# Kernel optimization log

Hardware: AMD Instinct MI355X
Metric: run time of the kernel (lower is better)

## Reference

```python
import jax, jax.numpy as jnp
import numpy as np

D_MODEL = 1024
HEADS = 16
Q_DIM = 1024
HEAD_DIM = Q_DIM // HEADS


def setup_inputs() -> dict:
    key = jax.random.key(0)
    ks = jax.random.split(key, 9)
    B, S = 2, 2048
    scale = 1.0 / np.sqrt(D_MODEL)
    inp = {
        "embeddings": jax.random.normal(ks[0], (B, S, D_MODEL), dtype=jnp.float32),
        "Wq": jax.random.normal(ks[1], (D_MODEL, Q_DIM), dtype=jnp.float32) * scale,
        "bq": jnp.zeros((Q_DIM,), dtype=jnp.float32),
        "Wk": jax.random.normal(ks[2], (D_MODEL, Q_DIM), dtype=jnp.float32) * scale,
        "bk": jnp.zeros((Q_DIM,), dtype=jnp.float32),
        "Wv": jax.random.normal(ks[3], (D_MODEL, Q_DIM), dtype=jnp.float32) * scale,
        "bv": jnp.zeros((Q_DIM,), dtype=jnp.float32),
        "Wo": jax.random.normal(ks[4], (Q_DIM, D_MODEL), dtype=jnp.float32) * scale,
        "bo": jnp.zeros((D_MODEL,), dtype=jnp.float32),
    }
    return inp


def reference(embeddings, Wq, bq, Wk, bk, Wv, bv, Wo, bo):
    B, S, _ = embeddings.shape
    # projections -> [B, H, S, Dh]
    def proj(W, b):
        x = embeddings @ W + b
        return x.reshape(B, S, HEADS, HEAD_DIM).transpose(0, 2, 1, 3)
    q = proj(Wq, bq)
    k = proj(Wk, bk)
    v = proj(Wv, bv)
    # scores scaled by sqrt(head_dim) as in source (no mask, dropout is no-op)
    scores = jnp.einsum("bhqd,bhkd->bhqk", q, k) / jnp.sqrt(
        jnp.asarray(HEAD_DIM, dtype=q.dtype)
    )
    p = jax.nn.softmax(scores, axis=-1)
    attn = jnp.einsum("bhqk,bhkd->bhqd", p, v)
    attn = attn.transpose(0, 2, 1, 3).reshape(B, S, Q_DIM)
    return attn @ Wo + bo
```

## Files before the change

### kernel.cpp

```cpp
#include <hip/hip_runtime.h>
#include <hip/hip_bf16.h>

#define BB 2
#define SS 2048
#define DMODEL 1024
#define NHEADS 16
#define DHEAD 64
#define MTOT (BB*SS)
#define NQKV 3072
#define QSCALE 0.18033688011112042f

typedef short bh8 __attribute__((ext_vector_type(8)));
typedef float fx4 __attribute__((ext_vector_type(4)));

__device__ __forceinline__ short f2bs(float f) {
    __hip_bfloat16 h = __float2bfloat16(f);
    return *reinterpret_cast<short*>(&h);
}

__device__ __forceinline__ void gload_lds16(const short* g, short* l) {
    __builtin_amdgcn_global_load_lds(
        (const __attribute__((address_space(1))) unsigned int*)g,
        (__attribute__((address_space(3))) unsigned int*)l, 16, 0, 0);
}

__global__ __launch_bounds__(256) void cvt_emb(const float* __restrict__ x,
                                               short* __restrict__ y, int n) {
    int i = (blockIdx.x * 256 + threadIdx.x) * 4;
    if (i + 3 < n) {
        float4 v = *(const float4*)(x + i);
        short4 o;
        o.x = f2bs(v.x); o.y = f2bs(v.y); o.z = f2bs(v.z); o.w = f2bs(v.w);
        *(short4*)(y + i) = o;
    }
}

__global__ __launch_bounds__(256) void transpose_w(
        const float* __restrict__ Wq, const float* __restrict__ Wk,
        const float* __restrict__ Wv, const float* __restrict__ Wo,
        short* __restrict__ Wt_qkv, short* __restrict__ Wot) {
    __shared__ float tile[64][65];
    int z = blockIdx.z;
    const float* src = (z == 0) ? Wq : (z == 1) ? Wk : (z == 2) ? Wv : Wo;
    short* dst = (z == 3) ? Wot : (Wt_qkv + (size_t)z * 1024 * 1024);
    int n0 = blockIdx.x * 64, k0 = blockIdx.y * 64;
    int tx = threadIdx.x, ty = threadIdx.y;
    for (int j = 0; j < 16; j++) {
        int r = ty + j * 4;
        tile[r][tx] = src[(size_t)(k0 + r) * 1024 + n0 + tx];
    }
    __syncthreads();
    for (int j = 0; j < 16; j++) {
        int r = ty + j * 4;
        dst[(size_t)(n0 + r) * 1024 + k0 + tx] = f2bs(tile[tx][r]);
    }
}

template<int BM, int BN, int NN, int MODE>
__global__ __launch_bounds__(256) void gemm_bt_t(
        const short* __restrict__ A, const short* __restrict__ Bt,
        const float* __restrict__ bq, const float* __restrict__ bk,
        const float* __restrict__ bv, const float* __restrict__ bo,
        short* __restrict__ Qout, short* __restrict__ Kout,
        short* __restrict__ Vtout, float* __restrict__ Cout) {
    const int K = 1024;
    constexpr int ROWS = BM + BN;
    constexpr int CPW  = ROWS / 64;
    constexpr int MBK  = MTOT / BM;
    constexpr int STRIP = MBK / 8;
    constexpr int MT = BM / 32, NT = BN / 32;
    __shared__ __align__(16) short S[3][ROWS * 32];

    int tid = threadIdx.x;
    int w = tid >> 6, l = tid & 63, quad = l >> 4, ln = l & 15;
    int wm = w & 1, wn = w >> 1;

    int id = blockIdx.x;
    int xcd = id & 7, local = id >> 3;
    int mi = xcd * STRIP + (local % STRIP);
    int ni = local / STRIP;
    int m0 = mi * BM, n0 = ni * BN;

    const short* gsrc[CPW];
    int loff[CPW];
    #pragma unroll
    for (int j = 0; j < CPW; j++) {
        int r0 = (w * CPW + j) * 16;
        int row = r0 + (l >> 2);
        gsrc[j] = (r0 < BM ? A + (size_t)(m0 + row) * K
                           : Bt + (size_t)(n0 + row - BM) * K) + (l & 3) * 8;
        loff[j] = r0 * 32;
    }

    short *sC = &S[0][0], *sN = &S[1][0], *sN2 = &S[2][0];
    #pragma unroll
    for (int j = 0; j < CPW; j++) gload_lds16(gsrc[j], sC + loff[j]);
    #pragma unroll
    for (int j = 0; j < CPW; j++) gload_lds16(gsrc[j] + 32, sN + loff[j]);

    fx4 acc[MT][NT] = {};
    for (int it = 0; it < 32; ++it) {
        if (it < 31) {
            if constexpr (CPW == 4)
                asm volatile("s_waitcnt vmcnt(4)\n\ts_barrier" ::: "memory");
            else
                asm volatile("s_waitcnt vmcnt(3)\n\ts_barrier" ::: "memory");
        } else {
            asm volatile("s_waitcnt vmcnt(0)\n\ts_barrier" ::: "memory");
        }
        if (it < 30) {
            int k0 = (it + 2) * 32;
            #pragma unroll
            for (int j = 0; j < CPW; j++) gload_lds16(gsrc[j] + k0, sN2 + loff[j]);
        }
        bh8 af[MT], bf[NT];
        #pragma unroll
        for (int mt = 0; mt < MT; mt++)
            af[mt] = *(const bh8*)&sC[(wm * (BM / 2) + mt * 16 + ln) * 32 + quad * 8];
        #pragma unroll
        for (int nt = 0; nt < NT; nt++)
            bf[nt] = *(const bh8*)&sC[(BM + wn * (BN / 2) + nt * 16 + ln) * 32 + quad * 8];
        #pragma unroll
        for (int mt = 0; mt < MT; mt++)
            #pragma unroll
            for (int nt = 0; nt < NT; nt++)
                acc[mt][nt] = __builtin_amdgcn_mfma_f32_16x16x32_bf16(af[mt], bf[nt], acc[mt][nt], 0, 0, 0);
        short* t;
        t = sC; sC = sN; sN = sN2; sN2 = t;
    }

    #pragma unroll
    for (int mt = 0; mt < MT; mt++) {
        #pragma unroll
        for (int nt = 0; nt < NT; nt++) {
            int n = n0 + wn * (BN / 2) + nt * 16 + ln;
            int mbase = m0 + wm * (BM / 2) + mt * 16 + quad * 4;
            #pragma unroll
            for (int r = 0; r < 4; r++) {
                float v = acc[mt][nt][r];
                int m = mbase + r;
                if constexpr (MODE == 0) {
                    int which = n >> 10, nn = n & 1023, h = nn >> 6, d = nn & 63;
                    float bias = (which == 0) ? bq[nn] : (which == 1) ? bk[nn] : bv[nn];
                    v += bias;
                    int b = m >> 11, s = m & 2047;
                    if (which == 0)
                        Qout[(((size_t)(b * 16 + h) * 2048) + s) * 64 + d] = f2bs(v * QSCALE);
                    else if (which == 1)
                        Kout[(((size_t)(b * 16 + h) * 2048) + s) * 64 + d] = f2bs(v);
                    else
                        Vtout[((size_t)(b * 16 + h) * 64 + d) * 2048 + s] = f2bs(v);
                } else {
                    Cout[(size_t)m * 1024 + n] = v + bo[n];
                }
            }
        }
    }
}

__global__ __launch_bounds__(256, 4) void flash_attn(
        const short* __restrict__ Q, const short* __restrict__ Kg,
        const short* __restrict__ Vt,
        float* __restrict__ O0, float* __restrict__ O1,
        float* __restrict__ L0, float* __restrict__ L1) {
    __shared__ __align__(16) short Ks[64 * 64];
    __shared__ __align__(16) short Vs[64 * 64];
    __shared__ __align__(16) short Ps[4][32 * 68];

    int tid = threadIdx.x;
    int w = tid >> 6, l = tid & 63, quad = l >> 4, ln = l & 15;
    int id = blockIdx.x;
    int xcd = id & 7, local = id >> 3;
    int bh = xcd * 4 + (local & 3);
    int t = local >> 2;
    int qx = t & 15, z = t >> 4;
    int qblk = qx * 128 + w * 32;
    const short* Qb = Q  + (size_t)bh * 2048 * 64;
    const short* Kb = Kg + (size_t)bh * 2048 * 64 + (size_t)z * 1024 * 64;
    const short* Vb = Vt + (size_t)bh * 64 * 2048 + z * 1024;
    float* Op = z ? O1 : O0;
    float* Lp = z ? L1 : L0;
    int swz = ln & 7;

    bh8 qf[2][2];
    #pragma unroll
    for (int qt = 0; qt < 2; qt++)
        #pragma unroll
        for (int c = 0; c < 2; c++)
            qf[qt][c] = *(const bh8*)&Qb[(size_t)(qblk + qt * 16 + ln) * 64 + c * 32 + quad * 8];

    int srow = tid >> 2, sp0 = tid & 3;
    int kw0 = srow * 64 + ((sp0 ^ (srow & 7)) * 8);
    int kw1 = srow * 64 + (((sp0 + 4) ^ (srow & 7)) * 8);
    const short* gK = Kb + (size_t)srow * 64;
    const short* gV = Vb + (size_t)srow * 2048;

    {
        uint4 a = *(const uint4*)(gK + sp0 * 8);
        uint4 bb = *(const uint4*)(gK + (sp0 + 4) * 8);
        uint4 c = *(const uint4*)(gV + sp0 * 8);
        uint4 d = *(const uint4*)(gV + (sp0 + 4) * 8);
        *(uint4*)&Ks[kw0] = a; *(uint4*)&Ks[kw1] = bb;
        *(uint4*)&Vs[kw0] = c; *(uint4*)&Vs[kw1] = d;
    }
    asm volatile("s_waitcnt lgkmcnt(0)\n\ts_barrier" ::: "memory");

    fx4 o[2][4] = {};
    float lpart[2] = {0.f, 0.f};

    for (int it = 0; it < 16; ++it) {
        uint4 ra, rb, rc, rd;
        bool pre = (it < 15);
        if (pre) {
            const short* gk = gK + (size_t)(it + 1) * 4096;
            const short* gv = gV + (size_t)(it + 1) * 64;
            ra = *(const uint4*)(gk + sp0 * 8);
            rb = *(const uint4*)(gk + (sp0 + 4) * 8);
            rc = *(const uint4*)(gv + sp0 * 8);
            rd = *(const uint4*)(gv + (sp0 + 4) * 8);
        }

        fx4 s[2][4] = {};
        #pragma unroll
        for (int mt = 0; mt < 4; mt++) {
            bh8 kf0 = *(const bh8*)&Ks[(mt * 16 + ln) * 64 + ((quad ^ swz) * 8)];
            bh8 kf1 = *(const bh8*)&Ks[(mt * 16 + ln) * 64 + (((quad + 4) ^ swz) * 8)];
            #pragma unroll
            for (int qt = 0; qt < 2; qt++) {
                s[qt][mt] = __builtin_amdgcn_mfma_f32_16x16x32_bf16(kf0, qf[qt][0], s[qt][mt], 0, 0, 0);
                s[qt][mt] = __builtin_amdgcn_mfma_f32_16x16x32_bf16(kf1, qf[qt][1], s[qt][mt], 0, 0, 0);
            }
        }

        #pragma unroll
        for (int qt = 0; qt < 2; qt++) {
            #pragma unroll
            for (int mt = 0; mt < 4; mt++) {
                float p0 = __builtin_amdgcn_exp2f(s[qt][mt][0]);
                float p1 = __builtin_amdgcn_exp2f(s[qt][mt][1]);
                float p2 = __builtin_amdgcn_exp2f(s[qt][mt][2]);
                float p3 = __builtin_amdgcn_exp2f(s[qt][mt][3]);
                lpart[qt] += (p0 + p1) + (p2 + p3);
                union { __hip_bfloat162 h2[2]; short4 s4; } u;
                u.h2[0] = __float22bfloat162_rn(make_float2(p0, p1));
                u.h2[1] = __float22bfloat162_rn(make_float2(p2, p3));
                *(short4*)&Ps[w][(qt * 16 + ln) * 64 +
                                 (((mt * 2 + (quad >> 1)) ^ swz) * 8) + (quad & 1) * 4] = u.s4;
            }
        }
        asm volatile("s_waitcnt lgkmcnt(0)" ::: "memory");

        #pragma unroll
        for (int c2 = 0; c2 < 2; c2++) {
            bh8 pf0 = *(const bh8*)&Ps[w][(0 * 16 + ln) * 64 + (((c2 * 4 + quad) ^ swz) * 8)];
            bh8 pf1 = *(const bh8*)&Ps[w][(1 * 16 + ln) * 64 + (((c2 * 4 + quad) ^ swz) * 8)];
            #pragma unroll
            for (int dt = 0; dt < 4; dt++) {
                bh8 vf = *(const bh8*)&Vs[(dt * 16 + ln) * 64 + (((c2 * 4 + quad) ^ swz) * 8)];
                o[0][dt] = __builtin_amdgcn_mfma_f32_16x16x32_bf16(vf, pf0, o[0][dt], 0, 0, 0);
                o[1][dt] = __builtin_amdgcn_mfma_f32_16x16x32_bf16(vf, pf1, o[1][dt], 0, 0, 0);
            }
        }

        asm volatile("s_barrier" ::: "memory");
        if (pre) {
            *(uint4*)&Ks[kw0] = ra; *(uint4*)&Ks[kw1] = rb;
            *(uint4*)&Vs[kw0] = rc; *(uint4*)&Vs[kw1] = rd;
        }
        asm volatile("s_waitcnt lgkmcnt(0)\n\ts_barrier" ::: "memory");
    }

    float* PsF = (float*)&Ps[w][0];
    int row = l >> 2, seg = l & 3;
    #pragma unroll
    for (int qt = 0; qt < 2; qt++) {
        #pragma unroll
        for (int dt = 0; dt < 4; dt++)
            *(fx4*)&PsF[ln * 68 + dt * 16 + quad * 4] = o[qt][dt];
        asm volatile("s_waitcnt lgkmcnt(0)" ::: "memory");
        float* orow = &Op[((size_t)bh * 2048 + qblk + qt * 16 + row) * 64];
        #pragma unroll
        for (int j = 0; j < 4; j++) {
            fx4 v = *(fx4*)&PsF[row * 68 + seg * 16 + j * 4];
            *(fx4*)&orow[seg * 16 + j * 4] = v;
        }
        asm volatile("s_waitcnt lgkmcnt(0)" ::: "memory");
        float lr = lpart[qt];
        lr += __shfl_xor(lr, 16);
        lr += __shfl_xor(lr, 32);
        if (l < 16) Lp[(size_t)bh * 2048 + qblk + qt * 16 + l] = lr;
    }
}

__global__ __launch_bounds__(256) void combine(
        const float* __restrict__ O0, const float* __restrict__ O1,
        const float* __restrict__ L0, const float* __restrict__ L1,
        short* __restrict__ Ctx) {
    int t = blockIdx.x * 256 + threadIdx.x;
    size_t base = (size_t)t * 8;
    int bhq = t >> 3;
    int d = (t & 7) * 8;
    int bh = bhq >> 11, q = bhq & 2047;
    int b = bh >> 4, h = bh & 15;
    float inv = 1.0f / (L0[bhq] + L1[bhq]);
    float4 a0 = *(const float4*)(O0 + base);
    float4 a1 = *(const float4*)(O0 + base + 4);
    float4 c0 = *(const float4*)(O1 + base);
    float4 c1 = *(const float4*)(O1 + base + 4);
    union { short s[8]; bh8 v; } o;
    o.s[0] = f2bs((a0.x + c0.x) * inv); o.s[1] = f2bs((a0.y + c0.y) * inv);
    o.s[2] = f2bs((a0.z + c0.z) * inv); o.s[3] = f2bs((a0.w + c0.w) * inv);
    o.s[4] = f2bs((a1.x + c1.x) * inv); o.s[5] = f2bs((a1.y + c1.y) * inv);
    o.s[6] = f2bs((a1.z + c1.z) * inv); o.s[7] = f2bs((a1.w + c1.w) * inv);
    *(bh8*)&Ctx[((size_t)(b * 2048 + q)) * 1024 + h * 64 + d] = o.v;
}

extern "C" void kernel_launch(void* const* d_in, const int* in_sizes, int n_in,
                              void* d_out, int out_size, void* d_ws, size_t ws_size,
                              hipStream_t stream) {
    const float* emb = (const float*)d_in[0];
    const float* Wq  = (const float*)d_in[1];
    const float* bq  = (const float*)d_in[2];
    const float* Wk  = (const float*)d_in[3];
    const float* bk  = (const float*)d_in[4];
    const float* Wv  = (const float*)d_in[5];
    const float* bv  = (const float*)d_in[6];
    const float* Wo  = (const float*)d_in[7];
    const float* bo  = (const float*)d_in[8];

    char* ws = (char*)d_ws;
    const size_t MB = 1024 * 1024;
    short* Xbf  = (short*)(ws + 0);
    short* Wt   = (short*)(ws + 8 * MB);
    float* Op1  = (float*)(ws + 0);
    short* Wot  = (short*)(ws + 17 * MB);
    short* Qb   = (short*)(ws + 19 * MB);
    short* Ctx  = (short*)(ws + 19 * MB);
    short* Kb   = (short*)(ws + 27 * MB);
    short* Vtb  = (short*)(ws + 35 * MB);
    float* L0   = (float*)(ws + 43 * MB);
    float* L1   = (float*)(ws + 43 * MB + 256 * 1024);
    float* Op0  = (float*)d_out;

    cvt_emb<<<4096, 256, 0, stream>>>(emb, Xbf, MTOT * DMODEL);
    transpose_w<<<dim3(16, 16, 4), dim3(64, 4), 0, stream>>>(Wq, Wk, Wv, Wo, Wt, Wot);
    gemm_bt_t<128, 128, NQKV, 0><<<768, 256, 0, stream>>>(
        Xbf, Wt, bq, bk, bv, nullptr, Qb, Kb, Vtb, nullptr);
    flash_attn<<<1024, 256, 0, stream>>>(Qb, Kb, Vtb, Op0, Op1, L0, L1);
    combine<<<2048, 256, 0, stream>>>(Op0, Op1, L0, L1, Ctx);
    gemm_bt_t<64, 128, DMODEL, 1><<<512, 256, 0, stream>>>(
        Ctx, Wot, nullptr, nullptr, nullptr, bo, nullptr, nullptr, nullptr, (float*)d_out);
}
```

Baseline: 207.7 us.

## Double-buffer K/V tiles with direct global-to-LDS loads in flash attention

Replaces the register-staged K/V prefetch with double-buffered LDS tiles filled by global_load_lds. Each wave loads its own 16 rows with a source-side XOR swizzle, so each iteration needs one vmcnt wait and barrier instead of two barriers plus register-to-LDS stores. V fragments are hoisted into registers before the softmax. The P staging buffer is halved by processing one 16-row query tile at a time. The epilogue reuses the K/V LDS region for output staging; this adds LDS footprint and register pressure, which may reduce occupancy.

```diff
diff --git a/kernel.cpp b/kernel.cpp
--- a/kernel.cpp
+++ b/kernel.cpp
@@ -163,9 +163,9 @@
         const short* __restrict__ Vt,
         float* __restrict__ O0, float* __restrict__ O1,
         float* __restrict__ L0, float* __restrict__ L1) {
-    __shared__ __align__(16) short Ks[64 * 64];
-    __shared__ __align__(16) short Vs[64 * 64];
-    __shared__ __align__(16) short Ps[4][32 * 68];
+    __shared__ __align__(16) short Ks[2][64 * 64];
+    __shared__ __align__(16) short Vs[2][64 * 64];
+    __shared__ __align__(16) short Ps[4][16 * 64];
 
     int tid = threadIdx.x;
     int w = tid >> 6, l = tid & 63, quad = l >> 4, ln = l & 15;
@@ -189,48 +189,55 @@
         for (int c = 0; c < 2; c++)
             qf[qt][c] = *(const bh8*)&Qb[(size_t)(qblk + qt * 16 + ln) * 64 + c * 32 + quad * 8];
 
-    int srow = tid >> 2, sp0 = tid & 3;
-    int kw0 = srow * 64 + ((sp0 ^ (srow & 7)) * 8);
-    int kw1 = srow * 64 + (((sp0 + 4) ^ (srow & 7)) * 8);
-    const short* gK = Kb + (size_t)srow * 64;
-    const short* gV = Vb + (size_t)srow * 2048;
-
-    {
-        uint4 a = *(const uint4*)(gK + sp0 * 8);
-        uint4 bb = *(const uint4*)(gK + (sp0 + 4) * 8);
-        uint4 c = *(const uint4*)(gV + sp0 * 8);
-        uint4 d = *(const uint4*)(gV + (sp0 + 4) * 8);
-        *(uint4*)&Ks[kw0] = a; *(uint4*)&Ks[kw1] = bb;
-        *(uint4*)&Vs[kw0] = c; *(uint4*)&Vs[kw1] = d;
-    }
-    asm volatile("s_waitcnt lgkmcnt(0)\n\ts_barrier" ::: "memory");
+    int r0 = w * 16;
+    int rowA = r0 + (l >> 3), rowB = rowA + 8;
+    int posn = l & 7;
+    const short* gKa = Kb + (size_t)rowA * 64   + ((posn ^ (rowA & 7)) * 8);
+    const short* gKc = Kb + (size_t)rowB * 64   + ((posn ^ (rowB & 7)) * 8);
+    const short* gVa = Vb + (size_t)rowA * 2048 + ((posn ^ (rowA & 7)) * 8);
+    const short* gVc = Vb + (size_t)rowB * 2048 + ((posn ^ (rowB & 7)) * 8);
+
+    gload_lds16(gKa, &Ks[0][r0 * 64]);
+    gload_lds16(gKc, &Ks[0][(r0 + 8) * 64]);
+    gload_lds16(gVa, &Vs[0][r0 * 64]);
+    gload_lds16(gVc, &Vs[0][(r0 + 8) * 64]);
 
     fx4 o[2][4] = {};
     float lpart[2] = {0.f, 0.f};
 
     for (int it = 0; it < 16; ++it) {
-        uint4 ra, rb, rc, rd;
-        bool pre = (it < 15);
-        if (pre) {
-            const short* gk = gK + (size_t)(it + 1) * 4096;
-            const short* gv = gV + (size_t)(it + 1) * 64;
-            ra = *(const uint4*)(gk + sp0 * 8);
-            rb = *(const uint4*)(gk + (sp0 + 4) * 8);
-            rc = *(const uint4*)(gv + sp0 * 8);
-            rd = *(const uint4*)(gv + (sp0 + 4) * 8);
-        }
+        asm volatile("s_waitcnt vmcnt(0)\n\ts_barrier" ::: "memory");
+        int cur = it & 1;
+        if (it < 15) {
+            int nb = cur ^ 1;
+            size_t ko = (size_t)(it + 1) * 4096;
+            size_t vo = (size_t)(it + 1) * 64;
+            gload_lds16(gKa + ko, &Ks[nb][r0 * 64]);
+            gload_lds16(gKc + ko, &Ks[nb][(r0 + 8) * 64]);
+            gload_lds16(gVa + vo, &Vs[nb][r0 * 64]);
+            gload_lds16(gVc + vo, &Vs[nb][(r0 + 8) * 64]);
+        }
+        const short* KsB = Ks[cur];
+        const short* VsB = Vs[cur];
 
         fx4 s[2][4] = {};
         #pragma unroll
         for (int mt = 0; mt < 4; mt++) {
-            bh8 kf0 = *(const bh8*)&Ks[(mt * 16 + ln) * 64 + ((quad ^ swz) * 8)];
-            bh8 kf1 = *(const bh8*)&Ks[(mt * 16 + ln) * 64 + (((quad + 4) ^ swz) * 8)];
+            bh8 kf0 = *(const bh8*)&KsB[(mt * 16 + ln) * 64 + ((quad ^ swz) * 8)];
+            bh8 kf1 = *(const bh8*)&KsB[(mt * 16 + ln) * 64 + (((quad + 4) ^ swz) * 8)];
             #pragma unroll
             for (int qt = 0; qt < 2; qt++) {
                 s[qt][mt] = __builtin_amdgcn_mfma_f32_16x16x32_bf16(kf0, qf[qt][0], s[qt][mt], 0, 0, 0);
                 s[qt][mt] = __builtin_amdgcn_mfma_f32_16x16x32_bf16(kf1, qf[qt][1], s[qt][mt], 0, 0, 0);
             }
         }
+
+        bh8 vf[2][4];
+        #pragma unroll
+        for (int c2 = 0; c2 < 2; c2++)
+            #pragma unroll
+            for (int dt = 0; dt < 4; dt++)
+                vf[c2][dt] = *(const bh8*)&VsB[(dt * 16 + ln) * 64 + (((c2 * 4 + quad) ^ swz) * 8)];
 
         #pragma unroll
         for (int qt = 0; qt < 2; qt++) {
@@ -244,33 +251,22 @@
                 union { __hip_bfloat162 h2[2]; short4 s4; } u;
                 u.h2[0] = __float22bfloat162_rn(make_float2(p0, p1));
                 u.h2[1] = __float22bfloat162_rn(make_float2(p2, p3));
-                *(short4*)&Ps[w][(qt * 16 + ln) * 64 +
+                *(short4*)&Ps[w][ln * 64 +
                                  (((mt * 2 + (quad >> 1)) ^ swz) * 8) + (quad & 1) * 4] = u.s4;
             }
-        }
-        asm volatile("s_waitcnt lgkmcnt(0)" ::: "memory");
-
-        #pragma unroll
-        for (int c2 = 0; c2 < 2; c2++) {
-            bh8 pf0 = *(const bh8*)&Ps[w][(0 * 16 + ln) * 64 + (((c2 * 4 + quad) ^ swz) * 8)];
-            bh8 pf1 = *(const bh8*)&Ps[w][(1 * 16 + ln) * 64 + (((c2 * 4 + quad) ^ swz) * 8)];
-            #pragma unroll
-            for (int dt = 0; dt < 4; dt++) {
-                bh8 vf = *(const bh8*)&Vs[(dt * 16 + ln) * 64 + (((c2 * 4 + quad) ^ swz) * 8)];
-                o[0][dt] = __builtin_amdgcn_mfma_f32_16x16x32_bf16(vf, pf0, o[0][dt], 0, 0, 0);
-                o[1][dt] = __builtin_amdgcn_mfma_f32_16x16x32_bf16(vf, pf1, o[1][dt], 0, 0, 0);
+            asm volatile("s_waitcnt lgkmcnt(0)" ::: "memory");
+            #pragma unroll
+            for (int c2 = 0; c2 < 2; c2++) {
+                bh8 pf = *(const bh8*)&Ps[w][ln * 64 + (((c2 * 4 + quad) ^ swz) * 8)];
+                #pragma unroll
+                for (int dt = 0; dt < 4; dt++)
+                    o[qt][dt] = __builtin_amdgcn_mfma_f32_16x16x32_bf16(vf[c2][dt], pf, o[qt][dt], 0, 0, 0);
             }
         }
-
-        asm volatile("s_barrier" ::: "memory");
-        if (pre) {
-            *(uint4*)&Ks[kw0] = ra; *(uint4*)&Ks[kw1] = rb;
-            *(uint4*)&Vs[kw0] = rc; *(uint4*)&Vs[kw1] = rd;
-        }
-        asm volatile("s_waitcnt lgkmcnt(0)\n\ts_barrier" ::: "memory");
-    }
-
-    float* PsF = (float*)&Ps[w][0];
+    }
+
+    asm volatile("s_barrier" ::: "memory");
+    float* PsF = (float*)&Ks[0][0] + w * 1088;
     int row = l >> 2, seg = l & 3;
     #pragma unroll
     for (int qt = 0; qt < 2; qt++) {
```

Result: slower. 222.6 us (+7.2%).
